# Kernel optimization log

Hardware: AMD Instinct MI355X
Metric: run time of the kernel (lower is better)

## Reference

```python
import jax, jax.numpy as jnp
import numpy as np
from jax import lax

D_MODEL = 1024
INTER = 1024
N_EXPERTS = 8
TOP_K = 2
ROUTE_SCALE = 1.0
B, S = 2, 4096


def setup_inputs() -> dict:
    key = jax.random.key(0)
    ks = jax.random.split(key, 16)
    sc_d = 1.0 / np.sqrt(D_MODEL)
    sc_f = 1.0 / np.sqrt(INTER)
    inp = {
        "x": jax.random.normal(ks[0], (B, S, D_MODEL), dtype=jnp.float32),
        "gate_w": jax.random.normal(ks[1], (N_EXPERTS, D_MODEL), dtype=jnp.float32) * sc_d,
        # stacked routed-expert SwiGLU params
        "w1": jax.random.normal(ks[2], (N_EXPERTS, D_MODEL, INTER), dtype=jnp.float32) * sc_d,
        "b1": jnp.zeros((N_EXPERTS, INTER), dtype=jnp.float32),
        "w2": jax.random.normal(ks[3], (N_EXPERTS, INTER, D_MODEL), dtype=jnp.float32) * sc_f,
        "b2": jnp.zeros((N_EXPERTS, D_MODEL), dtype=jnp.float32),
        "w3": jax.random.normal(ks[4], (N_EXPERTS, D_MODEL, INTER), dtype=jnp.float32) * sc_d,
        "b3": jnp.zeros((N_EXPERTS, INTER), dtype=jnp.float32),
        # shared expert (dense MLP on all tokens)
        "sw1": jax.random.normal(ks[5], (D_MODEL, INTER), dtype=jnp.float32) * sc_d,
        "sb1": jnp.zeros((INTER,), dtype=jnp.float32),
        "sw2": jax.random.normal(ks[6], (INTER, D_MODEL), dtype=jnp.float32) * sc_f,
        "sb2": jnp.zeros((D_MODEL,), dtype=jnp.float32),
        "sw3": jax.random.normal(ks[7], (D_MODEL, INTER), dtype=jnp.float32) * sc_d,
        "sb3": jnp.zeros((INTER,), dtype=jnp.float32),
    }
    return inp


def reference(x, gate_w, w1, b1, w2, b2, w3, b3, sw1, sb1, sw2, sb2, sw3, sb3):
    Bx, Sx, D = x.shape
    xt = x.reshape(-1, D)  # [T, D]

    # --- Gate: softmax scores, top-k experts (n_groups==1, no bias branch) ---
    scores = jax.nn.softmax((xt @ gate_w.T).astype(jnp.float32), axis=-1)  # [T, E]
    top_vals, top_idx = lax.top_k(scores, TOP_K)  # [T, K]
    weights = (top_vals * ROUTE_SCALE).astype(x.dtype)  # gather of original scores == top_vals

    # combine[t, e] = sum_k weights[t, k] * (top_idx[t, k] == e)
    combine = jnp.sum(
        jax.nn.one_hot(top_idx, N_EXPERTS, dtype=x.dtype) * weights[..., None], axis=1
    )  # [T, E]

    # --- Routed experts: scan over experts, weighted accumulate ---
    def body(acc, p):
        W1, B1, W2, B2, W3, B3, c = p  # c: [T] combine weights for this expert
        h = jax.nn.silu(xt @ W1 + B1) * (xt @ W3 + B3)  # [T, INTER]
        return acc + c[:, None] * (h @ W2 + B2), None

    y, _ = lax.scan(body, jnp.zeros_like(xt), (w1, b1, w2, b2, w3, b3, combine.T))

    # --- Shared expert on all tokens ---
    z = (jax.nn.silu(xt @ sw1 + sb1) * (xt @ sw3 + sb3)) @ sw2 + sb2

    return (y + z).reshape(Bx, Sx, D)
```

## Files before the change

### kernel.cpp

```cpp
#include <hip/hip_runtime.h>
#include <hip/hip_bf16.h>
#include <math.h>

#define D_MODEL 1024
#define INTER   1024
#define NEXP    8
#define T_TOK   8192
#define ROWCAP  17408

typedef short  short8 __attribute__((ext_vector_type(8)));
typedef float  f32x4  __attribute__((ext_vector_type(4)));

__device__ __forceinline__ ushort f2bf(float f) {
    uint u = __float_as_uint(f);
    u += 0x7fffu + ((u >> 16) & 1u);
    return (ushort)(u >> 16);
}
__device__ __forceinline__ float bf2f(ushort u) {
    return __uint_as_float((uint)u << 16);
}
__device__ __forceinline__ uint pk2(float lo, float hi) {
    return (uint)f2bf(lo) | ((uint)f2bf(hi) << 16);
}
__device__ __forceinline__ void gll16(const ushort* g, ushort* l) {
    __builtin_amdgcn_global_load_lds(
        (const __attribute__((address_space(1))) unsigned int*)(g),
        (__attribute__((address_space(3))) unsigned int*)(l), 16, 0, 0);
}

#define IDX64(r, c) ((r) * 64 + (((c) ^ ((r) & 7)) * 8))

__global__ __launch_bounds__(256)
void k_xbf(const float* __restrict__ X, ushort* __restrict__ Xb)
{
    const size_t i = ((size_t)blockIdx.x * 256 + threadIdx.x) * 8;
    float4 a = *(const float4*)(X + i);
    float4 b = *(const float4*)(X + i + 4);
    uint4 o = { pk2(a.x, a.y), pk2(a.z, a.w), pk2(b.x, b.y), pk2(b.z, b.w) };
    *(uint4*)(Xb + i) = o;
}

__global__ __launch_bounds__(256)
void k_gate(const float* __restrict__ X, const float* __restrict__ GW,
            int* __restrict__ topk_idx, float* __restrict__ topk_w,
            int* __restrict__ cnt)
{
    __shared__ int lcnt[NEXP];
    const int t = threadIdx.x;
    if (t < NEXP) lcnt[t] = 0;
    const int lane = t & 63, wv = t >> 6;
    float4 gwr[NEXP][4];
#pragma unroll
    for (int e = 0; e < NEXP; ++e)
#pragma unroll
        for (int i = 0; i < 4; ++i)
            gwr[e][i] = *(const float4*)(GW + e * 1024 + i * 256 + lane * 4);
    __syncthreads();
    const int tok0 = blockIdx.x * 32 + wv * 8;
    const bool b0 = lane & 1, b1 = lane & 2, b2 = lane & 4;
    for (int tt = 0; tt < 8; ++tt) {
        const int tok = tok0 + tt;
        const float* xr = X + (size_t)tok * 1024;
        float4 xv[4];
#pragma unroll
        for (int i = 0; i < 4; ++i) xv[i] = *(const float4*)(xr + i * 256 + lane * 4);
        float p[NEXP];
#pragma unroll
        for (int e = 0; e < NEXP; ++e) {
            float s = 0.f;
#pragma unroll
            for (int i = 0; i < 4; ++i)
                s += xv[i].x * gwr[e][i].x + xv[i].y * gwr[e][i].y
                   + xv[i].z * gwr[e][i].z + xv[i].w * gwr[e][i].w;
            p[e] = s;
        }
        float q[4];
#pragma unroll
        for (int j = 0; j < 4; ++j) {
            float send = b0 ? p[j] : p[j + 4];
            float recv = __shfl_xor(send, 1, 64);
            q[j] = (b0 ? p[j + 4] : p[j]) + recv;
        }
        float u2[2];
#pragma unroll
        for (int j = 0; j < 2; ++j) {
            float send = b1 ? q[j] : q[j + 2];
            float recv = __shfl_xor(send, 2, 64);
            u2[j] = (b1 ? q[j + 2] : q[j]) + recv;
        }
        float send = b2 ? u2[0] : u2[1];
        float r = (b2 ? u2[1] : u2[0]) + __shfl_xor(send, 4, 64);
        r += __shfl_xor(r, 8, 64);
        r += __shfl_xor(r, 16, 64);
        r += __shfl_xor(r, 32, 64);
        float sc[NEXP];
#pragma unroll
        for (int e = 0; e < NEXP; ++e)
            sc[e] = __shfl(r, ((e & 1) << 2) | (e & 2) | ((e >> 2) & 1), 64);
        float m = sc[0];
#pragma unroll
        for (int e = 1; e < NEXP; ++e) m = fmaxf(m, sc[e]);
        float ssum = 0.f;
#pragma unroll
        for (int e = 0; e < NEXP; ++e) { sc[e] = __expf(sc[e] - m); ssum += sc[e]; }
        float inv = 1.f / ssum;
#pragma unroll
        for (int e = 0; e < NEXP; ++e) sc[e] *= inv;
        int i0 = 0; float v0 = sc[0];
#pragma unroll
        for (int e = 1; e < NEXP; ++e) if (sc[e] > v0) { v0 = sc[e]; i0 = e; }
        int i1 = -1; float v1 = -1e30f;
#pragma unroll
        for (int e = 0; e < NEXP; ++e) if (e != i0 && sc[e] > v1) { v1 = sc[e]; i1 = e; }
        if (lane == 0) {
            topk_idx[2 * tok]     = i0;
            topk_idx[2 * tok + 1] = i1;
            topk_w[2 * tok]       = v0;
            topk_w[2 * tok + 1]   = v1;
            atomicAdd(&lcnt[i0], 1);
            atomicAdd(&lcnt[i1], 1);
        }
    }
    __syncthreads();
    if (t < NEXP) atomicAdd(&cnt[t], lcnt[t]);
}

__global__ void k_prefix(const int* __restrict__ cnt, int* __restrict__ offs)
{
    if (threadIdx.x == 0 && blockIdx.x == 0) {
        int tot = 0;
        for (int e = 0; e < NEXP; ++e) {
            offs[e] = tot;
            tot += ((cnt[e] + 127) / 128) * 128;
        }
        offs[NEXP] = tot;
    }
}

__global__ void k_scatter(const int* __restrict__ topk_idx, const float* __restrict__ topk_w,
                          const int* __restrict__ offs, int* __restrict__ cnt2,
                          int* __restrict__ rowid, float* __restrict__ rowwt,
                          int* __restrict__ rowslot)
{
    __shared__ int loc[NEXP];
    __shared__ int base[NEXP];
    const int t = threadIdx.x;
    if (t < NEXP) loc[t] = 0;
    __syncthreads();
    const int tok = blockIdx.x * 256 + t;
    const int e0 = topk_idx[2 * tok], e1 = topk_idx[2 * tok + 1];
    const int s0 = atomicAdd(&loc[e0], 1);
    const int s1 = atomicAdd(&loc[e1], 1);
    __syncthreads();
    if (t < NEXP) base[t] = atomicAdd(&cnt2[t], loc[t]);
    __syncthreads();
    int p0 = offs[e0] + base[e0] + s0;
    rowid[p0] = tok; rowwt[p0] = topk_w[2 * tok]; rowslot[p0] = 0;
    int p1 = offs[e1] + base[e1] + s1;
    rowid[p1] = tok; rowwt[p1] = topk_w[2 * tok + 1]; rowslot[p1] = 1;
}

__global__ __launch_bounds__(256)
void k_tw(const float* __restrict__ srcA, ushort* __restrict__ dstA,
          const float* __restrict__ srcB, ushort* __restrict__ dstB, int nA)
{
    __shared__ float tl[64][132];
    int m = blockIdx.y;
    const float* src; ushort* dst;
    if (m < nA) { src = srcA + ((size_t)m << 20); dst = dstA + ((size_t)m << 20); }
    else { m -= nA;  src = srcB + ((size_t)m << 20); dst = dstB + ((size_t)m << 20); }
    const int tile = blockIdx.x;
    const int nb = tile >> 4, kt = tile & 15;
    const int t = threadIdx.x;
    const int c4 = (t & 31) * 4, kr = t >> 5;
#pragma unroll
    for (int i = 0; i < 8; ++i) {
        const int kl = kr + 8 * i;
        float4 v = *(const float4*)(src + (size_t)(kt * 64 + kl) * 1024 + nb * 128 + c4);
        tl[kl][c4 + 0] = v.x; tl[kl][c4 + 1] = v.y;
        tl[kl][c4 + 2] = v.z; tl[kl][c4 + 3] = v.w;
    }
    __syncthreads();
    const int nl = t >> 1, h = t & 1;
    ushort* drow = dst + (size_t)tile * 8192 + nl * 64;
#pragma unroll
    for (int w = 0; w < 4; ++w) {
        const int cimg = h * 4 + w;
        const int cl = cimg ^ (nl & 7);
        float f[8];
#pragma unroll
        for (int j = 0; j < 8; ++j) f[j] = tl[cl * 8 + j][nl];
        uint4 o = { pk2(f[0], f[1]), pk2(f[2], f[3]), pk2(f[4], f[5]), pk2(f[6], f[7]) };
        *(uint4*)(drow + cimg * 8) = o;
    }
}

template <bool ROUTED, bool AA>
__global__ __launch_bounds__(256, 2)
void k_h(const float* __restrict__ X, const ushort* __restrict__ Xb,
         const ushort* __restrict__ W1t, const float* __restrict__ B1,
         const ushort* __restrict__ W3t, const float* __restrict__ B3,
         ushort* __restrict__ Hb,
         const int* __restrict__ rowid, const int* __restrict__ offs,
         const int* __restrict__ cnt)
{
    __shared__ __align__(16) ushort As [128 * 64];
    __shared__ __align__(16) ushort B1s[128 * 64];
    __shared__ __align__(16) ushort B3s[128 * 64];
    __shared__ int ridc[128];

    const int nbx  = blockIdx.x;
    const int nb   = nbx * 128;
    const int row0 = blockIdx.y * 128;

    int rstart = 0, rcount = T_TOK;
    const ushort* w1 = W1t; const ushort* w3 = W3t;
    if constexpr (ROUTED) {
        const int total = offs[NEXP];
        if (row0 >= total) return;
        int e = 0;
        while (offs[e + 1] <= row0) ++e;
        rstart = offs[e]; rcount = cnt[e];
        w1 += (size_t)e << 20; B1 += e * INTER;
        w3 += (size_t)e << 20; B3 += e * INTER;
    }
    const int t = threadIdx.x;
    const ushort* g1 = w1 + (size_t)(nbx * 16) * 8192 + t * 8;
    const ushort* g3 = w3 + (size_t)(nbx * 16) * 8192 + t * 8;

    const ushort* asrc[4];
    const float*  Ap = nullptr;
    int aoff[4];
    if constexpr (AA) {
        if constexpr (ROUTED) {
            if (t < 128) {
                const int rr = row0 + t;
                ridc[t] = ((rr - rstart) < rcount) ? rowid[rr] : 0;
            }
            __syncthreads();
        }
        const int sub = t >> 3, ci = t & 7;
#pragma unroll
        for (int c = 0; c < 4; ++c) {
            const int r = c * 32 + sub;
            const int tok = ROUTED ? ridc[r] : (row0 + r);
            asrc[c] = Xb + (size_t)tok * 1024 + (size_t)((ci ^ (sub & 7)) * 8);
        }
    } else {
        const int arow = t >> 1, ah = t & 1;
        int atok;
        if constexpr (ROUTED) {
            bool valid = (row0 + arow - rstart) < rcount;
            atok = valid ? rowid[row0 + arow] : 0;
        } else {
            atok = row0 + arow;
        }
        Ap = X + (size_t)atok * D_MODEL + ah * 32;
#pragma unroll
        for (int w = 0; w < 4; ++w) aoff[w] = IDX64(arow, ah * 4 + w);
    }

    const int lane = t & 63, wid = t >> 6;
    const int wm = wid & 1, wn = wid >> 1;
    const int m16 = lane & 15, g = lane >> 4;
    int offA[2][4], offB[2][4];
#pragma unroll
    for (int ks = 0; ks < 2; ++ks)
#pragma unroll
        for (int i = 0; i < 4; ++i) {
            offA[ks][i] = IDX64(wm * 64 + i * 16 + m16, ks * 4 + g);
            offB[ks][i] = IDX64(wn * 64 + i * 16 + m16, ks * 4 + g);
        }

    const f32x4 zf = {0.f, 0.f, 0.f, 0.f};
    f32x4 acc1[4][4], acc3[4][4];
#pragma unroll
    for (int i = 0; i < 4; ++i)
#pragma unroll
        for (int j = 0; j < 4; ++j) { acc1[i][j] = zf; acc3[i][j] = zf; }

    for (int kt = 0; kt < 16; ++kt) {
        if constexpr (AA) {
            __syncthreads();
#pragma unroll
            for (int c = 0; c < 4; ++c)
                gll16(asrc[c] + kt * 64, &As[c * 2048 + t * 8]);
#pragma unroll
            for (int c = 0; c < 4; ++c) {
                gll16(g1 + kt * 8192 + c * 2048, &B1s[c * 2048 + t * 8]);
                gll16(g3 + kt * 8192 + c * 2048, &B3s[c * 2048 + t * 8]);
            }
            __syncthreads();
        } else {
            float4 av[8];
#pragma unroll
            for (int w = 0; w < 8; ++w) av[w] = *(const float4*)(Ap + kt * 64 + w * 4);
            __syncthreads();
#pragma unroll
            for (int c = 0; c < 4; ++c) {
                gll16(g1 + kt * 8192 + c * 2048, &B1s[c * 2048 + t * 8]);
                gll16(g3 + kt * 8192 + c * 2048, &B3s[c * 2048 + t * 8]);
            }
#pragma unroll
            for (int w = 0; w < 4; ++w) {
                uint4 aw = { pk2(av[2*w].x, av[2*w].y),     pk2(av[2*w].z, av[2*w].w),
                             pk2(av[2*w+1].x, av[2*w+1].y), pk2(av[2*w+1].z, av[2*w+1].w) };
                *(uint4*)&As[aoff[w]] = aw;
            }
            __syncthreads();
        }
#pragma unroll
        for (int ks = 0; ks < 2; ++ks) {
            short8 af[4], b1f[4], b3f[4];
#pragma unroll
            for (int i = 0; i < 4; ++i) {
                af[i]  = *(const short8*)&As [offA[ks][i]];
                b1f[i] = *(const short8*)&B1s[offB[ks][i]];
                b3f[i] = *(const short8*)&B3s[offB[ks][i]];
            }
#pragma unroll
            for (int i = 0; i < 4; ++i)
#pragma unroll
                for (int j = 0; j < 4; ++j) {
                    acc1[i][j] = __builtin_amdgcn_mfma_f32_16x16x32_bf16(af[i], b1f[j], acc1[i][j], 0, 0, 0);
                    acc3[i][j] = __builtin_amdgcn_mfma_f32_16x16x32_bf16(af[i], b3f[j], acc3[i][j], 0, 0, 0);
                }
        }
    }

#pragma unroll
    for (int j = 0; j < 4; ++j) {
        const int gcol = nb + wn * 64 + j * 16 + m16;
        const float bb1 = B1[gcol];
        const float bb3 = B3[gcol];
#pragma unroll
        for (int i = 0; i < 4; ++i) {
            const int growb = row0 + wm * 64 + i * 16 + g * 4;
#pragma unroll
            for (int r = 0; r < 4; ++r) {
                float x1 = acc1[i][j][r] + bb1;
                float x3 = acc3[i][j][r] + bb3;
                float h = x1 / (1.f + __expf(-x1)) * x3;
                Hb[(size_t)(growb + r) * INTER + gcol] = f2bf(h);
            }
        }
    }
}

template <int MODE>
__global__ __launch_bounds__(256, 2)
void k_out(const ushort* __restrict__ Hin,
           const ushort* __restrict__ W2t, const float* __restrict__ B2,
           float* __restrict__ out,
           const int* __restrict__ rowid, const int* __restrict__ offs,
           const int* __restrict__ cnt, const float* __restrict__ rowwt,
           const int* __restrict__ rowslot, ushort* __restrict__ Yb)
{
    __shared__ __align__(16) ushort As[128 * 64];
    __shared__ __align__(16) ushort Bs[128 * 64];

    const int nbx  = blockIdx.x;
    const int nb   = nbx * 128;
    const int row0 = blockIdx.y * 128;

    int rstart = 0, rcount = T_TOK;
    const ushort* w2 = W2t;
    if constexpr (MODE != 0) {
        const int total = offs[NEXP];
        if (row0 >= total) return;
        int e = 0;
        while (offs[e + 1] <= row0) ++e;
        rstart = offs[e]; rcount = cnt[e];
        w2 += (size_t)e << 20; B2 += e * D_MODEL;
    }
    const int t = threadIdx.x;
    const ushort* g2 = w2 + (size_t)(nbx * 16) * 8192 + t * 8;

    const int sub = t >> 3, ci = t & 7;
    const ushort* asrc[4];
#pragma unroll
    for (int c = 0; c < 4; ++c) {
        const int r = c * 32 + sub;
        asrc[c] = Hin + (size_t)(row0 + r) * 1024 + (size_t)((ci ^ (sub & 7)) * 8);
    }

    const int lane = t & 63, wid = t >> 6;
    const int wm = wid & 1, wn = wid >> 1;
    const int m16 = lane & 15, g = lane >> 4;
    int offA[2][4], offB[2][4];
#pragma unroll
    for (int ks = 0; ks < 2; ++ks)
#pragma unroll
        for (int i = 0; i < 4; ++i) {
            offA[ks][i] = IDX64(wm * 64 + i * 16 + m16, ks * 4 + g);
            offB[ks][i] = IDX64(wn * 64 + i * 16 + m16, ks * 4 + g);
        }

    const f32x4 zf = {0.f, 0.f, 0.f, 0.f};
    f32x4 acc[4][4];
#pragma unroll
    for (int i = 0; i < 4; ++i)
#pragma unroll
        for (int j = 0; j < 4; ++j) acc[i][j] = zf;

    for (int kt = 0; kt < 16; ++kt) {
        __syncthreads();
#pragma unroll
        for (int c = 0; c < 4; ++c)
            gll16(asrc[c] + kt * 64, &As[c * 2048 + t * 8]);
#pragma unroll
        for (int c = 0; c < 4; ++c)
            gll16(g2 + kt * 8192 + c * 2048, &Bs[c * 2048 + t * 8]);
        __syncthreads();
#pragma unroll
        for (int ks = 0; ks < 2; ++ks) {
            short8 af[4], bf[4];
#pragma unroll
            for (int i = 0; i < 4; ++i) {
                af[i] = *(const short8*)&As[offA[ks][i]];
                bf[i] = *(const short8*)&Bs[offB[ks][i]];
            }
#pragma unroll
            for (int i = 0; i < 4; ++i)
#pragma unroll
                for (int j = 0; j < 4; ++j)
                    acc[i][j] = __builtin_amdgcn_mfma_f32_16x16x32_bf16(af[i], bf[j], acc[i][j], 0, 0, 0);
        }
    }

#pragma unroll
    for (int i = 0; i < 4; ++i) {
#pragma unroll
        for (int r = 0; r < 4; ++r) {
            const int grow = row0 + wm * 64 + i * 16 + g * 4 + r;
            if constexpr (MODE == 0) {
#pragma unroll
                for (int j = 0; j < 4; ++j) {
                    const int gcol = nb + wn * 64 + j * 16 + m16;
                    out[(size_t)grow * D_MODEL + gcol] = acc[i][j][r] + B2[gcol];
                }
            } else {
                const bool valid = (grow - rstart) < rcount;
                if (!valid) continue;
                const int tok = rowid[grow];
                const float wt = rowwt[grow];
                if constexpr (MODE == 1) {
#pragma unroll
                    for (int j = 0; j < 4; ++j) {
                        const int gcol = nb + wn * 64 + j * 16 + m16;
                        atomicAdd(out + (size_t)tok * D_MODEL + gcol,
                                  wt * (acc[i][j][r] + B2[gcol]));
                    }
                } else {
                    const int sk = rowslot[grow];
                    ushort* yr = Yb + (((size_t)sk * T_TOK + tok) << 10);
#pragma unroll
                    for (int j = 0; j < 4; ++j) {
                        const int gcol = nb + wn * 64 + j * 16 + m16;
                        yr[gcol] = f2bf(wt * (acc[i][j][r] + B2[gcol]));
                    }
                }
            }
        }
    }
}

__global__ __launch_bounds__(256)
void k_combine(float* __restrict__ out, const ushort* __restrict__ Yb)
{
    const int row = blockIdx.x;
    const int c = threadIdx.x * 4;
    float4 o = *(const float4*)(out + (size_t)row * 1024 + c);
    ushort4 y0 = *(const ushort4*)(Yb + (size_t)row * 1024 + c);
    ushort4 y1 = *(const ushort4*)(Yb + ((size_t)(T_TOK + row)) * 1024 + c);
    o.x += bf2f(y0.x) + bf2f(y1.x);
    o.y += bf2f(y0.y) + bf2f(y1.y);
    o.z += bf2f(y0.z) + bf2f(y1.z);
    o.w += bf2f(y0.w) + bf2f(y1.w);
    *(float4*)(out + (size_t)row * 1024 + c) = o;
}

extern "C" void kernel_launch(void* const* d_in, const int* in_sizes, int n_in,
                              void* d_out, int out_size, void* d_ws, size_t ws_size,
                              hipStream_t stream)
{
    const float* x   = (const float*)d_in[0];
    const float* gw  = (const float*)d_in[1];
    const float* w1  = (const float*)d_in[2];
    const float* b1  = (const float*)d_in[3];
    const float* w2  = (const float*)d_in[4];
    const float* b2  = (const float*)d_in[5];
    const float* w3  = (const float*)d_in[6];
    const float* b3  = (const float*)d_in[7];
    const float* sw1 = (const float*)d_in[8];
    const float* sb1 = (const float*)d_in[9];
    const float* sw2 = (const float*)d_in[10];
    const float* sb2 = (const float*)d_in[11];
    const float* sw3 = (const float*)d_in[12];
    const float* sb3 = (const float*)d_in[13];
    float* out = (float*)d_out;

    char* ws = (char*)d_ws;
    int*   cnt      = (int*)(ws);
    int*   cnt2     = (int*)(ws + 64);
    int*   offs     = (int*)(ws + 128);
    int*   topk_idx = (int*)(ws + 256);
    float* topk_w   = (float*)(ws + 256 + 65536);
    int*   rowid    = (int*)(ws + 256 + 131072);
    float* rowwt    = (float*)(ws + 256 + 131072 + ROWCAP * 4);
    int*   rowslot  = (int*)(ws + 256 + 131072 + ROWCAP * 8);
    ushort* Hb = (ushort*)(ws + 524288);
    ushort* WA = (ushort*)(ws + 524288 + (size_t)ROWCAP * 2048);
    ushort* WB = WA + (8u << 20);
    ushort* WC = WB + (8u << 20);
    const bool bigws = ws_size >= (size_t)86507520;

    ushort* sw1t = WB;
    ushort* sw3t = WB + (1 << 20);
    ushort* sw2t = WA;
    ushort* w1t  = WA;
    ushort* w3t  = WB;
    ushort* w2t  = bigws ? WC : WA;
    ushort* Xbf  = WC;
    ushort* Yb   = WA;

    hipMemsetAsync(ws, 0, 256, stream);

    k_gate<<<256, 256, 0, stream>>>(x, gw, topk_idx, topk_w, cnt);
    k_prefix<<<1, 64, 0, stream>>>(cnt, offs);
    k_scatter<<<32, 256, 0, stream>>>(topk_idx, topk_w, offs, cnt2, rowid, rowwt, rowslot);

    if (bigws) {
        k_xbf<<<4096, 256, 0, stream>>>(x, Xbf);

        k_tw<<<dim3(128, 2), 256, 0, stream>>>(sw1, sw1t, sw3, sw3t, 1);
        k_h<false, true><<<dim3(8, 64), 256, 0, stream>>>(x, Xbf, sw1t, sb1, sw3t, sb3, Hb,
                                                          nullptr, nullptr, nullptr);
        k_tw<<<dim3(128, 1), 256, 0, stream>>>(sw2, sw2t, sw2, sw2t, 1);
        k_out<0><<<dim3(8, 64), 256, 0, stream>>>(Hb, sw2t, sb2, out,
                                                  nullptr, nullptr, nullptr, nullptr,
                                                  nullptr, nullptr);

        k_tw<<<dim3(128, 16), 256, 0, stream>>>(w1, w1t, w3, w3t, 8);
        k_h<true, true><<<dim3(8, ROWCAP / 128), 256, 0, stream>>>(x, Xbf, w1t, b1, w3t, b3, Hb,
                                                                   rowid, offs, cnt);
        k_tw<<<dim3(128, 8), 256, 0, stream>>>(w2, w2t, w2, w2t, 8);
        k_out<2><<<dim3(8, ROWCAP / 128), 256, 0, stream>>>(Hb, w2t, b2, out,
                                                            rowid, offs, cnt, rowwt,
                                                            rowslot, Yb);
        k_combine<<<T_TOK, 256, 0, stream>>>(out, Yb);
    } else {
        k_tw<<<dim3(128, 2), 256, 0, stream>>>(sw1, sw1t, sw3, sw3t, 1);
        k_h<false, false><<<dim3(8, 64), 256, 0, stream>>>(x, nullptr, sw1t, sb1, sw3t, sb3, Hb,
                                                           nullptr, nullptr, nullptr);
        k_tw<<<dim3(128, 1), 256, 0, stream>>>(sw2, sw2t, sw2, sw2t, 1);
        k_out<0><<<dim3(8, 64), 256, 0, stream>>>(Hb, sw2t, sb2, out,
                                                  nullptr, nullptr, nullptr, nullptr,
                                                  nullptr, nullptr);
        k_tw<<<dim3(128, 16), 256, 0, stream>>>(w1, w1t, w3, w3t, 8);
        k_h<true, false><<<dim3(8, ROWCAP / 128), 256, 0, stream>>>(x, nullptr, w1t, b1, w3t, b3, Hb,
                                                                    rowid, offs, cnt);
        k_tw<<<dim3(128, 8), 256, 0, stream>>>(w2, w2t, w2, w2t, 8);
        k_out<1><<<dim3(8, ROWCAP / 128), 256, 0, stream>>>(Hb, w2t, b2, out,
                                                            rowid, offs, cnt, rowwt,
                                                            rowslot, Yb);
    }
}
```

Before: 446.6 us.

## Interleave W1/W3 columns into one matrix and double-buffer LDS in GEMMs

A new transpose kernel interleaves W1 and W3 columns into one bf16 matrix, so the gate-up kernel runs a single 128-wide GEMM per block (half the N per block, twice the blocks). The epilogue pairs adjacent lanes with a shuffle to form silu(x1)*x3. Both the up and down GEMMs now double-buffer LDS, prefetching the next K tile while MFMAs run on the current one. The cost is more LDS per block, which may lower occupancy, and twice as many gate-up blocks, each re-reading the A tile.

```diff
diff --git a/kernel.cpp b/kernel.cpp
--- a/kernel.cpp
+++ b/kernel.cpp
@@ -195,55 +195,89 @@
     }
 }
 
+__global__ __launch_bounds__(256)
+void k_twi(const float* __restrict__ s1, const float* __restrict__ s3,
+           ushort* __restrict__ dst)
+{
+    __shared__ float tl1[64][68];
+    __shared__ float tl3[64][68];
+    const int m = blockIdx.y;
+    const float* p1 = s1 + ((size_t)m << 20);
+    const float* p3 = s3 + ((size_t)m << 20);
+    ushort* d = dst + ((size_t)m << 21);
+    const int tile = blockIdx.x;
+    const int nb = tile >> 4, kt = tile & 15;
+    const int t = threadIdx.x;
+    const int c4 = (t & 15) * 4, kr = t >> 4;
+#pragma unroll
+    for (int i = 0; i < 4; ++i) {
+        const int kl = kr + 16 * i;
+        float4 v1 = *(const float4*)(p1 + (size_t)(kt * 64 + kl) * 1024 + nb * 64 + c4);
+        float4 v3 = *(const float4*)(p3 + (size_t)(kt * 64 + kl) * 1024 + nb * 64 + c4);
+        tl1[kl][c4 + 0] = v1.x; tl1[kl][c4 + 1] = v1.y;
+        tl1[kl][c4 + 2] = v1.z; tl1[kl][c4 + 3] = v1.w;
+        tl3[kl][c4 + 0] = v3.x; tl3[kl][c4 + 1] = v3.y;
+        tl3[kl][c4 + 2] = v3.z; tl3[kl][c4 + 3] = v3.w;
+    }
+    __syncthreads();
+    const int nl = t >> 1, h = t & 1;
+    const int rc = nl >> 1;
+    const float (*tt)[68] = (nl & 1) ? tl3 : tl1;
+    ushort* drow = d + (size_t)tile * 8192 + nl * 64;
+#pragma unroll
+    for (int w = 0; w < 4; ++w) {
+        const int cimg = h * 4 + w;
+        const int cl = cimg ^ (nl & 7);
+        float f[8];
+#pragma unroll
+        for (int j = 0; j < 8; ++j) f[j] = tt[cl * 8 + j][rc];
+        uint4 o = { pk2(f[0], f[1]), pk2(f[2], f[3]), pk2(f[4], f[5]), pk2(f[6], f[7]) };
+        *(uint4*)(drow + cimg * 8) = o;
+    }
+}
+
 template <bool ROUTED, bool AA>
 __global__ __launch_bounds__(256, 2)
 void k_h(const float* __restrict__ X, const ushort* __restrict__ Xb,
-         const ushort* __restrict__ W1t, const float* __restrict__ B1,
-         const ushort* __restrict__ W3t, const float* __restrict__ B3,
-         ushort* __restrict__ Hb,
+         const ushort* __restrict__ W13, const float* __restrict__ B1,
+         const float* __restrict__ B3, ushort* __restrict__ Hb,
          const int* __restrict__ rowid, const int* __restrict__ offs,
          const int* __restrict__ cnt)
 {
-    __shared__ __align__(16) ushort As [128 * 64];
-    __shared__ __align__(16) ushort B1s[128 * 64];
-    __shared__ __align__(16) ushort B3s[128 * 64];
-    __shared__ int ridc[128];
+    __shared__ __align__(16) ushort As[2][8192];
+    __shared__ __align__(16) ushort Bs[2][8192];
 
     const int nbx  = blockIdx.x;
-    const int nb   = nbx * 128;
     const int row0 = blockIdx.y * 128;
 
     int rstart = 0, rcount = T_TOK;
-    const ushort* w1 = W1t; const ushort* w3 = W3t;
+    const ushort* w = W13;
     if constexpr (ROUTED) {
         const int total = offs[NEXP];
         if (row0 >= total) return;
         int e = 0;
         while (offs[e + 1] <= row0) ++e;
         rstart = offs[e]; rcount = cnt[e];
-        w1 += (size_t)e << 20; B1 += e * INTER;
-        w3 += (size_t)e << 20; B3 += e * INTER;
+        w += (size_t)e << 21; B1 += e * INTER; B3 += e * INTER;
     }
     const int t = threadIdx.x;
-    const ushort* g1 = w1 + (size_t)(nbx * 16) * 8192 + t * 8;
-    const ushort* g3 = w3 + (size_t)(nbx * 16) * 8192 + t * 8;
+    const ushort* gB = w + (size_t)(nbx * 16) * 8192 + t * 8;
 
     const ushort* asrc[4];
     const float*  Ap = nullptr;
     int aoff[4];
     if constexpr (AA) {
-        if constexpr (ROUTED) {
-            if (t < 128) {
-                const int rr = row0 + t;
-                ridc[t] = ((rr - rstart) < rcount) ? rowid[rr] : 0;
-            }
-            __syncthreads();
-        }
         const int sub = t >> 3, ci = t & 7;
 #pragma unroll
         for (int c = 0; c < 4; ++c) {
             const int r = c * 32 + sub;
-            const int tok = ROUTED ? ridc[r] : (row0 + r);
+            int tok;
+            if constexpr (ROUTED) {
+                bool valid = (row0 + r - rstart) < rcount;
+                tok = valid ? rowid[row0 + r] : 0;
+            } else {
+                tok = row0 + r;
+            }
             asrc[c] = Xb + (size_t)tok * 1024 + (size_t)((ci ^ (sub & 7)) * 8);
         }
     } else {
@@ -257,7 +291,7 @@
         }
         Ap = X + (size_t)atok * D_MODEL + ah * 32;
 #pragma unroll
-        for (int w = 0; w < 4; ++w) aoff[w] = IDX64(arow, ah * 4 + w);
+        for (int w2 = 0; w2 < 4; ++w2) aoff[w2] = IDX64(arow, ah * 4 + w2);
     }
 
     const int lane = t & 63, wid = t >> 6;
@@ -273,75 +307,79 @@
         }
 
     const f32x4 zf = {0.f, 0.f, 0.f, 0.f};
-    f32x4 acc1[4][4], acc3[4][4];
+    f32x4 acc[4][4];
 #pragma unroll
     for (int i = 0; i < 4; ++i)
 #pragma unroll
-        for (int j = 0; j < 4; ++j) { acc1[i][j] = zf; acc3[i][j] = zf; }
-
+        for (int j = 0; j < 4; ++j) acc[i][j] = zf;
+
+    if constexpr (AA) {
+#pragma unroll
+        for (int c = 0; c < 4; ++c) gll16(asrc[c], &As[0][c * 2048 + t * 8]);
+    }
+#pragma unroll
+    for (int c = 0; c < 4; ++c) gll16(gB + c * 2048, &Bs[0][c * 2048 + t * 8]);
+
+    int cur = 0;
     for (int kt = 0; kt < 16; ++kt) {
-        if constexpr (AA) {
+        float4 av[8];
+        if constexpr (!AA) {
+#pragma unroll
+            for (int w2 = 0; w2 < 8; ++w2) av[w2] = *(const float4*)(Ap + kt * 64 + w2 * 4);
+        }
+        __syncthreads();
+        if (kt < 15) {
+            if constexpr (AA) {
+#pragma unroll
+                for (int c = 0; c < 4; ++c)
+                    gll16(asrc[c] + (kt + 1) * 64, &As[cur ^ 1][c * 2048 + t * 8]);
+            }
+#pragma unroll
+            for (int c = 0; c < 4; ++c)
+                gll16(gB + (size_t)(kt + 1) * 8192 + c * 2048, &Bs[cur ^ 1][c * 2048 + t * 8]);
+        }
+        if constexpr (!AA) {
+#pragma unroll
+            for (int w2 = 0; w2 < 4; ++w2) {
+                uint4 aw = { pk2(av[2*w2].x, av[2*w2].y),     pk2(av[2*w2].z, av[2*w2].w),
+                             pk2(av[2*w2+1].x, av[2*w2+1].y), pk2(av[2*w2+1].z, av[2*w2+1].w) };
+                *(uint4*)&As[cur][aoff[w2]] = aw;
+            }
             __syncthreads();
-#pragma unroll
-            for (int c = 0; c < 4; ++c)
-                gll16(asrc[c] + kt * 64, &As[c * 2048 + t * 8]);
-#pragma unroll
-            for (int c = 0; c < 4; ++c) {
-                gll16(g1 + kt * 8192 + c * 2048, &B1s[c * 2048 + t * 8]);
-                gll16(g3 + kt * 8192 + c * 2048, &B3s[c * 2048 + t * 8]);
-            }
-            __syncthreads();
-        } else {
-            float4 av[8];
-#pragma unroll
-            for (int w = 0; w < 8; ++w) av[w] = *(const float4*)(Ap + kt * 64 + w * 4);
-            __syncthreads();
-#pragma unroll
-            for (int c = 0; c < 4; ++c) {
-                gll16(g1 + kt * 8192 + c * 2048, &B1s[c * 2048 + t * 8]);
-                gll16(g3 + kt * 8192 + c * 2048, &B3s[c * 2048 + t * 8]);
-            }
-#pragma unroll
-            for (int w = 0; w < 4; ++w) {
-                uint4 aw = { pk2(av[2*w].x, av[2*w].y),     pk2(av[2*w].z, av[2*w].w),
-                             pk2(av[2*w+1].x, av[2*w+1].y), pk2(av[2*w+1].z, av[2*w+1].w) };
-                *(uint4*)&As[aoff[w]] = aw;
-            }
-            __syncthreads();
         }
 #pragma unroll
         for (int ks = 0; ks < 2; ++ks) {
-            short8 af[4], b1f[4], b3f[4];
+            short8 af[4], bf[4];
 #pragma unroll
             for (int i = 0; i < 4; ++i) {
-                af[i]  = *(const short8*)&As [offA[ks][i]];
-                b1f[i] = *(const short8*)&B1s[offB[ks][i]];
-                b3f[i] = *(const short8*)&B3s[offB[ks][i]];
+                af[i] = *(const short8*)&As[cur][offA[ks][i]];
+                bf[i] = *(const short8*)&Bs[cur][offB[ks][i]];
             }
 #pragma unroll
             for (int i = 0; i < 4; ++i)
 #pragma unroll
-                for (int j = 0; j < 4; ++j) {
-                    acc1[i][j] = __builtin_amdgcn_mfma_f32_16x16x32_bf16(af[i], b1f[j], acc1[i][j], 0, 0, 0);
-                    acc3[i][j] = __builtin_amdgcn_mfma_f32_16x16x32_bf16(af[i], b3f[j], acc3[i][j], 0, 0, 0);
-                }
-        }
+                for (int j = 0; j < 4; ++j)
+                    acc[i][j] = __builtin_amdgcn_mfma_f32_16x16x32_bf16(af[i], bf[j], acc[i][j], 0, 0, 0);
+        }
+        cur ^= 1;
     }
 
 #pragma unroll
     for (int j = 0; j < 4; ++j) {
-        const int gcol = nb + wn * 64 + j * 16 + m16;
-        const float bb1 = B1[gcol];
-        const float bb3 = B3[gcol];
+        const int p = nbx * 64 + wn * 32 + j * 8 + (m16 >> 1);
+        const float bb = (m16 & 1) ? B3[p] : B1[p];
 #pragma unroll
         for (int i = 0; i < 4; ++i) {
             const int growb = row0 + wm * 64 + i * 16 + g * 4;
 #pragma unroll
             for (int r = 0; r < 4; ++r) {
-                float x1 = acc1[i][j][r] + bb1;
-                float x3 = acc3[i][j][r] + bb3;
+                float tv = acc[i][j][r] + bb;
+                float pv = __shfl_xor(tv, 1, 64);
+                float x1 = (m16 & 1) ? pv : tv;
+                float x3 = (m16 & 1) ? tv : pv;
                 float h = x1 / (1.f + __expf(-x1)) * x3;
-                Hb[(size_t)(growb + r) * INTER + gcol] = f2bf(h);
+                if ((m16 & 1) == 0)
+                    Hb[(size_t)(growb + r) * INTER + p] = f2bf(h);
             }
         }
     }
@@ -356,8 +394,8 @@
            const int* __restrict__ cnt, const float* __restrict__ rowwt,
            const int* __restrict__ rowslot, ushort* __restrict__ Yb)
 {
-    __shared__ __align__(16) ushort As[128 * 64];
-    __shared__ __align__(16) ushort Bs[128 * 64];
+    __shared__ __align__(16) ushort As[2][8192];
+    __shared__ __align__(16) ushort Bs[2][8192];
 
     const int nbx  = blockIdx.x;
     const int nb   = nbx * 128;
@@ -403,22 +441,29 @@
 #pragma unroll
         for (int j = 0; j < 4; ++j) acc[i][j] = zf;
 
+#pragma unroll
+    for (int c = 0; c < 4; ++c) {
+        gll16(asrc[c], &As[0][c * 2048 + t * 8]);
+        gll16(g2 + c * 2048, &Bs[0][c * 2048 + t * 8]);
+    }
+
+    int cur = 0;
     for (int kt = 0; kt < 16; ++kt) {
         __syncthreads();
-#pragma unroll
-        for (int c = 0; c < 4; ++c)
-            gll16(asrc[c] + kt * 64, &As[c * 2048 + t * 8]);
-#pragma unroll
-        for (int c = 0; c < 4; ++c)
-            gll16(g2 + kt * 8192 + c * 2048, &Bs[c * 2048 + t * 8]);
-        __syncthreads();
+        if (kt < 15) {
+#pragma unroll
+            for (int c = 0; c < 4; ++c) {
+                gll16(asrc[c] + (kt + 1) * 64, &As[cur ^ 1][c * 2048 + t * 8]);
+                gll16(g2 + (size_t)(kt + 1) * 8192 + c * 2048, &Bs[cur ^ 1][c * 2048 + t * 8]);
+            }
+        }
 #pragma unroll
         for (int ks = 0; ks < 2; ++ks) {
             short8 af[4], bf[4];
 #pragma unroll
             for (int i = 0; i < 4; ++i) {
-                af[i] = *(const short8*)&As[offA[ks][i]];
-                bf[i] = *(const short8*)&Bs[offB[ks][i]];
+                af[i] = *(const short8*)&As[cur][offA[ks][i]];
+                bf[i] = *(const short8*)&Bs[cur][offB[ks][i]];
             }
 #pragma unroll
             for (int i = 0; i < 4; ++i)
@@ -426,6 +471,7 @@
                 for (int j = 0; j < 4; ++j)
                     acc[i][j] = __builtin_amdgcn_mfma_f32_16x16x32_bf16(af[i], bf[j], acc[i][j], 0, 0, 0);
         }
+        cur ^= 1;
     }
 
 #pragma unroll
@@ -515,14 +561,12 @@
     ushort* WC = WB + (8u << 20);
     const bool bigws = ws_size >= (size_t)86507520;
 
-    ushort* sw1t = WB;
-    ushort* sw3t = WB + (1 << 20);
-    ushort* sw2t = WA;
-    ushort* w1t  = WA;
-    ushort* w3t  = WB;
-    ushort* w2t  = bigws ? WC : WA;
-    ushort* Xbf  = WC;
-    ushort* Yb   = WA;
+    ushort* sw13t = WB;
+    ushort* sw2t  = WA;
+    ushort* w13t  = WA;
+    ushort* w2t   = bigws ? WC : WA;
+    ushort* Xbf   = WC;
+    ushort* Yb    = WA;
 
     hipMemsetAsync(ws, 0, 256, stream);
 
@@ -533,33 +577,33 @@
     if (bigws) {
         k_xbf<<<4096, 256, 0, stream>>>(x, Xbf);
 
-        k_tw<<<dim3(128, 2), 256, 0, stream>>>(sw1, sw1t, sw3, sw3t, 1);
-        k_h<false, true><<<dim3(8, 64), 256, 0, stream>>>(x, Xbf, sw1t, sb1, sw3t, sb3, Hb,
-                                                          nullptr, nullptr, nullptr);
+        k_twi<<<dim3(256, 1), 256, 0, stream>>>(sw1, sw3, sw13t);
+        k_h<false, true><<<dim3(16, 64), 256, 0, stream>>>(x, Xbf, sw13t, sb1, sb3, Hb,
+                                                           nullptr, nullptr, nullptr);
         k_tw<<<dim3(128, 1), 256, 0, stream>>>(sw2, sw2t, sw2, sw2t, 1);
         k_out<0><<<dim3(8, 64), 256, 0, stream>>>(Hb, sw2t, sb2, out,
                                                   nullptr, nullptr, nullptr, nullptr,
                                                   nullptr, nullptr);
 
-        k_tw<<<dim3(128, 16), 256, 0, stream>>>(w1, w1t, w3, w3t, 8);
-        k_h<true, true><<<dim3(8, ROWCAP / 128), 256, 0, stream>>>(x, Xbf, w1t, b1, w3t, b3, Hb,
-                                                                   rowid, offs, cnt);
+        k_twi<<<dim3(256, 8), 256, 0, stream>>>(w1, w3, w13t);
+        k_h<true, true><<<dim3(16, ROWCAP / 128), 256, 0, stream>>>(x, Xbf, w13t, b1, b3, Hb,
+                                                                    rowid, offs, cnt);
         k_tw<<<dim3(128, 8), 256, 0, stream>>>(w2, w2t, w2, w2t, 8);
         k_out<2><<<dim3(8, ROWCAP / 128), 256, 0, stream>>>(Hb, w2t, b2, out,
                                                             rowid, offs, cnt, rowwt,
                                                             rowslot, Yb);
         k_combine<<<T_TOK, 256, 0, stream>>>(out, Yb);
     } else {
-        k_tw<<<dim3(128, 2), 256, 0, stream>>>(sw1, sw1t, sw3, sw3t, 1);
-        k_h<false, false><<<dim3(8, 64), 256, 0, stream>>>(x, nullptr, sw1t, sb1, sw3t, sb3, Hb,
-                                                           nullptr, nullptr, nullptr);
+        k_twi<<<dim3(256, 1), 256, 0, stream>>>(sw1, sw3, sw13t);
+        k_h<false, false><<<dim3(16, 64), 256, 0, stream>>>(x, nullptr, sw13t, sb1, sb3, Hb,
+                                                            nullptr, nullptr, nullptr);
         k_tw<<<dim3(128, 1), 256, 0, stream>>>(sw2, sw2t, sw2, sw2t, 1);
         k_out<0><<<dim3(8, 64), 256, 0, stream>>>(Hb, sw2t, sb2, out,
                                                   nullptr, nullptr, nullptr, nullptr,
                                                   nullptr, nullptr);
-        k_tw<<<dim3(128, 16), 256, 0, stream>>>(w1, w1t, w3, w3t, 8);
-        k_h<true, false><<<dim3(8, ROWCAP / 128), 256, 0, stream>>>(x, nullptr, w1t, b1, w3t, b3, Hb,
-                                                                    rowid, offs, cnt);
+        k_twi<<<dim3(256, 8), 256, 0, stream>>>(w1, w3, w13t);
+        k_h<true, false><<<dim3(16, ROWCAP / 128), 256, 0, stream>>>(x, nullptr, w13t, b1, b3, Hb,
+                                                                     rowid, offs, cnt);
         k_tw<<<dim3(128, 8), 256, 0, stream>>>(w2, w2t, w2, w2t, 8);
         k_out<1><<<dim3(8, ROWCAP / 128), 256, 0, stream>>>(Hb, w2t, b2, out,
                                                             rowid, offs, cnt, rowwt,
```

Result: slower. 521.4 us (+16.7%).
